# Kernel tuning notes

Hardware: AMD Instinct MI355X
Metric: run time of the kernel (lower is better)

Reference implementation:

```python
import jax, jax.numpy as jnp
import numpy as np

N_USER = 250_000
N_ITEM = 250_000
E = 500_000
IN, H, C = 128, 64, 2
NEG_SLOPE = 0.01  # torch F.leaky_relu default


def setup_inputs() -> dict:
    key = jax.random.key(0)
    ks = jax.random.split(key, 24)
    d = {}
    d["feat_user"] = jax.random.normal(ks[0], (N_USER, IN), jnp.float32)
    d["feat_item"] = jax.random.normal(ks[1], (N_ITEM, IN), jnp.float32)
    # per-etype linear params, layer 1 (in_feats -> h_dim)
    s1 = 1.0 / np.sqrt(IN)
    d["W1_follows"] = jax.random.normal(ks[2], (IN, H), jnp.float32) * s1
    d["b1_follows"] = jax.random.normal(ks[3], (H,), jnp.float32) * s1
    d["W1_clicks"]  = jax.random.normal(ks[4], (IN, H), jnp.float32) * s1
    d["b1_clicks"]  = jax.random.normal(ks[5], (H,), jnp.float32) * s1
    d["W1_rev"]     = jax.random.normal(ks[6], (IN, H), jnp.float32) * s1
    d["b1_rev"]     = jax.random.normal(ks[7], (H,), jnp.float32) * s1
    # per-etype linear params, layer 2 (h_dim -> num_classes)
    s2 = 1.0 / np.sqrt(H)
    d["W2_follows"] = jax.random.normal(ks[8], (H, C), jnp.float32) * s2
    d["b2_follows"] = jax.random.normal(ks[9], (C,), jnp.float32) * s2
    d["W2_clicks"]  = jax.random.normal(ks[10], (H, C), jnp.float32) * s2
    d["b2_clicks"]  = jax.random.normal(ks[11], (C,), jnp.float32) * s2
    d["W2_rev"]     = jax.random.normal(ks[12], (H, C), jnp.float32) * s2
    d["b2_rev"]     = jax.random.normal(ks[13], (C,), jnp.float32) * s2
    # edge lists: (src, dst) per canonical etype
    d["follows_src"] = jax.random.randint(ks[14], (E,), 0, N_USER, jnp.int32)  # user->user
    d["follows_dst"] = jax.random.randint(ks[15], (E,), 0, N_USER, jnp.int32)
    d["clicks_src"]  = jax.random.randint(ks[16], (E,), 0, N_USER, jnp.int32)  # user->item
    d["clicks_dst"]  = jax.random.randint(ks[17], (E,), 0, N_ITEM, jnp.int32)
    d["rev_src"]     = jax.random.randint(ks[18], (E,), 0, N_ITEM, jnp.int32)  # item->user
    d["rev_dst"]     = jax.random.randint(ks[19], (E,), 0, N_USER, jnp.int32)
    return d


def _mean_agg(Wh, src, dst, n_dst):
    # copy_u + mean: gather transformed src feats per edge, segment-mean onto dst
    m = Wh[src]                                                   # [E, d]
    s = jax.ops.segment_sum(m, dst, num_segments=n_dst)           # [n_dst, d]
    deg = jax.ops.segment_sum(jnp.ones_like(dst, Wh.dtype), dst, num_segments=n_dst)
    return s / jnp.maximum(deg, 1.0)[:, None]                     # 0 for deg-0 nodes (DGL fills 0)


def _layer(fu, fi, Wf, bf, Wc, bc, Wr, br,
           fsrc, fdst, csrc, cdst, rsrc, rdst):
    # per-etype linear on src features, per-etype mean, cross-etype 'sum'
    h_user = (_mean_agg(fu @ Wf + bf, fsrc, fdst, N_USER)
              + _mean_agg(fi @ Wr + br, rsrc, rdst, N_USER))
    h_item = _mean_agg(fu @ Wc + bc, csrc, cdst, N_ITEM)
    return h_user, h_item


def reference(feat_user, feat_item,
              W1_follows, b1_follows, W1_clicks, b1_clicks, W1_rev, b1_rev,
              W2_follows, b2_follows, W2_clicks, b2_clicks, W2_rev, b2_rev,
              follows_src, follows_dst, clicks_src, clicks_dst, rev_src, rev_dst):
    h1u, h1i = _layer(feat_user, feat_item,
                      W1_follows, b1_follows, W1_clicks, b1_clicks, W1_rev, b1_rev,
                      follows_src, follows_dst, clicks_src, clicks_dst, rev_src, rev_dst)
    h2u = jnp.where(h1u >= 0, h1u, NEG_SLOPE * h1u)
    h2i = jnp.where(h1i >= 0, h1i, NEG_SLOPE * h1i)
    out_u, out_i = _layer(h2u, h2i,
                          W2_follows, b2_follows, W2_clicks, b2_clicks, W2_rev, b2_rev,
                          follows_src, follows_dst, clicks_src, clicks_dst, rev_src, rev_dst)
    # (h_dict, h_dict_2) flattened per ntype
    return (out_u, out_i, h2u, h2i)
```

## Files before the change

### kernel.cpp

```cpp
#include <hip/hip_runtime.h>
#include <cstdio>

#define NU 250000
#define NI 250000
#define NE 500000
#define ND 250000
#define NB_SCAN 245
#define NR 8
#define RSZ 31250

typedef __attribute__((ext_vector_type(8))) short short8v;
typedef __attribute__((ext_vector_type(4))) float float4v;

__device__ inline unsigned short f2bf(float x) {
  unsigned int b = __float_as_uint(x);
  unsigned int r = (b + 0x7FFFu + ((b >> 16) & 1u)) >> 16;
  return (unsigned short)r;
}
__device__ inline float bf2f(unsigned short u) {
  return __uint_as_float(((unsigned int)u) << 16);
}

__device__ inline void async_copy16(const float* g, float* l) {
  __builtin_amdgcn_global_load_lds((const __attribute__((address_space(1))) void*)g,
                                   (__attribute__((address_space(3))) void*)l, 16, 0, 0);
}

__device__ inline void nt_store4(float* p, float a, float b, float c, float d) {
  float4v v; v.x = a; v.y = b; v.z = c; v.w = d;
  __builtin_nontemporal_store(v, (float4v*)p);
}

__global__ void hist3_kernel(const int* __restrict__ fdst, const int* __restrict__ cdst,
                             const int* __restrict__ rdst,
                             int* __restrict__ degf, int* __restrict__ degc, int* __restrict__ degr) {
  int i = blockIdx.x * blockDim.x + threadIdx.x;
  if (i < NE) {
    atomicAdd(&degf[fdst[i]], 1);
    atomicAdd(&degc[cdst[i]], 1);
    atomicAdd(&degr[rdst[i]], 1);
  }
}

__global__ void scan1_kernel(const int* __restrict__ deg0, const int* __restrict__ deg1,
                             const int* __restrict__ deg2, int* __restrict__ bsum) {
  const int* deg = blockIdx.y == 0 ? deg0 : (blockIdx.y == 1 ? deg1 : deg2);
  int* bs = bsum + blockIdx.y * 256;
  __shared__ int s[256];
  int b = blockIdx.x, t = threadIdx.x;
  int base = b * 1024 + t * 4;
  int v = 0;
  #pragma unroll
  for (int i = 0; i < 4; ++i) if (base + i < ND) v += deg[base + i];
  s[t] = v; __syncthreads();
  for (int off = 128; off > 0; off >>= 1) { if (t < off) s[t] += s[t + off]; __syncthreads(); }
  if (t == 0) bs[b] = s[0];
}

__global__ void scan3_kernel(const int* __restrict__ deg0, const int* __restrict__ deg1,
                             const int* __restrict__ deg2, const int* __restrict__ bsum,
                             int* __restrict__ offs0, int* __restrict__ offs1, int* __restrict__ offs2,
                             int* __restrict__ cur0, int* __restrict__ cur1, int* __restrict__ cur2) {
  int y = blockIdx.y;
  const int* deg = y == 0 ? deg0 : (y == 1 ? deg1 : deg2);
  int* offs = y == 0 ? offs0 : (y == 1 ? offs1 : offs2);
  int* cursor = y == 0 ? cur0 : (y == 1 ? cur1 : cur2);
  const int* bs = bsum + y * 256;
  __shared__ int sb[256];
  __shared__ int s[256];
  int b = blockIdx.x, t = threadIdx.x;

  sb[t] = (t < NB_SCAN) ? bs[t] : 0;
  __syncthreads();
  for (int off = 1; off < 256; off <<= 1) {
    int x = (t >= off) ? sb[t - off] : 0;
    __syncthreads();
    sb[t] += x;
    __syncthreads();
  }
  int blockbase = (b == 0) ? 0 : sb[b - 1];

  int base = b * 1024 + t * 4;
  int v[4]; int sum = 0;
  #pragma unroll
  for (int i = 0; i < 4; ++i) { v[i] = (base + i < ND) ? deg[base + i] : 0; sum += v[i]; }
  s[t] = sum; __syncthreads();
  for (int off = 1; off < 256; off <<= 1) {
    int x = (t >= off) ? s[t - off] : 0;
    __syncthreads();
    s[t] += x;
    __syncthreads();
  }
  int run = blockbase + s[t] - sum;
  #pragma unroll
  for (int i = 0; i < 4; ++i) {
    if (base + i < ND) { offs[base + i] = run; cursor[base + i] = run; run += v[i]; }
  }
  if (b == 0 && t == 0) offs[ND] = NE;
}

__global__ void bucket_part_kernel(const int* __restrict__ fsrc, const int* __restrict__ fdst,
                                   const int* __restrict__ csrc, const int* __restrict__ cdst,
                                   const int* __restrict__ rsrc, const int* __restrict__ rdst,
                                   int* __restrict__ curf, int* __restrict__ curc, int* __restrict__ curr,
                                   int* __restrict__ srtf, int* __restrict__ srtc, int* __restrict__ srtr) {
  const int r = blockIdx.x & (NR - 1);
  const int chunk = blockIdx.x >> 3;
  const int lo = r * RSZ, hi = lo + RSZ;
  const int base = chunk * 1024;
  #pragma unroll
  for (int i = 0; i < 4; ++i) {
    int e = base + i * 256 + threadIdx.x;
    if (e < NE) {
      int d0 = fdst[e]; int s0 = fsrc[e];
      if (d0 >= lo && d0 < hi) { int p = atomicAdd(&curf[d0], 1); srtf[p] = s0; }
      int d1 = cdst[e]; int s1 = csrc[e];
      if (d1 >= lo && d1 < hi) { int p = atomicAdd(&curc[d1], 1); srtc[p] = s1; }
      int d2 = rdst[e]; int s2 = rsrc[e];
      if (d2 >= lo && d2 < hi) { int p = atomicAdd(&curr[d2], 1); srtr[p] = s2; }
    }
  }
}

__global__ void prepw_kernel(const float* __restrict__ W0, const float* __restrict__ W1,
                             const float* __restrict__ W2, unsigned short* __restrict__ T) {
  int gt = blockIdx.x * 256 + threadIdx.x;
  int et = gt >> 10;
  int g = gt & 1023;
  int gl = g & 63;
  int jm = (g >> 6) & 3;
  int c = g >> 8;
  int kb = c * 32 + (gl >> 4) * 8;
  int col = jm * 16 + (gl & 15);
  const float* W = et == 0 ? W0 : (et == 1 ? W1 : W2);
  short8v u;
  #pragma unroll
  for (int i = 0; i < 8; ++i) u[i] = (short)f2bf(W[(kb + i) * 64 + col]);
  ((short8v*)T)[gt] = u;
}

template <bool TWO>
__device__ inline void gemm_persist(float (*sx)[64 * 128],
                                    const float* __restrict__ X, int n, int ntiles,
                                    const unsigned short* __restrict__ Ta, const float* __restrict__ ba,
                                    const unsigned short* __restrict__ Tb, const float* __restrict__ bb,
                                    unsigned short* __restrict__ Ya, unsigned short* __restrict__ Yb) {
  const int tid = threadIdx.x;
  const int lane = tid & 63;
  const int wave = tid >> 6;
  const int cb = (lane >> 4) * 4;

  short8v A[4][4], B[4][4];
  #pragma unroll
  for (int c = 0; c < 4; ++c) {
    #pragma unroll
    for (int jm = 0; jm < 4; ++jm) {
      A[c][jm] = ((const short8v*)Ta)[c * 256 + jm * 64 + lane];
      if constexpr (TWO) B[c][jm] = ((const short8v*)Tb)[c * 256 + jm * 64 + lane];
    }
  }
  float4 bias_a[4], bias_b[4];
  #pragma unroll
  for (int jm = 0; jm < 4; ++jm) {
    bias_a[jm] = *(const float4*)&ba[jm * 16 + cb];
    if constexpr (TWO) bias_b[jm] = *(const float4*)&bb[jm * 16 + cb];
  }

  const int nl = wave * 16 + (lane & 15);
  const int sw = nl & 7;

  int t = blockIdx.x;
  if (t >= ntiles) return;
  {
    #pragma unroll
    for (int j = 0; j < 8; ++j) {
      int idx = (wave * 8 + j) * 64 + lane;
      int row = idx >> 5, u = idx & 31;
      int gr = t * 64 + row; if (gr >= n) gr = n - 1;
      const float* src = X + (size_t)gr * 128 + ((u ^ (row & 7)) << 2);
      float* dst = &sx[0][(wave * 8 + j) * 256];
      async_copy16(src, dst);
    }
  }
  asm volatile("s_waitcnt vmcnt(0)" ::: "memory");
  __syncthreads();

  int cur = 0;
  while (true) {
    int tn = t + (int)gridDim.x;
    bool more = (tn < ntiles);
    if (more) {
      #pragma unroll
      for (int j = 0; j < 8; ++j) {
        int idx = (wave * 8 + j) * 64 + lane;
        int row = idx >> 5, u = idx & 31;
        int gr = tn * 64 + row; if (gr >= n) gr = n - 1;
        const float* src = X + (size_t)gr * 128 + ((u ^ (row & 7)) << 2);
        float* dst = &sx[cur ^ 1][(wave * 8 + j) * 256];
        async_copy16(src, dst);
      }
    }

    float4v accA[4] = {};
    float4v accB[4] = {};
    #pragma unroll
    for (int c = 0; c < 4; ++c) {
      int s0 = c * 8 + (lane >> 4) * 2;
      float4 f0 = *(const float4*)&sx[cur][nl * 128 + (((s0 + 0) ^ sw) << 2)];
      float4 f1 = *(const float4*)&sx[cur][nl * 128 + (((s0 + 1) ^ sw) << 2)];
      short8v bfr;
      bfr[0] = (short)f2bf(f0.x); bfr[1] = (short)f2bf(f0.y);
      bfr[2] = (short)f2bf(f0.z); bfr[3] = (short)f2bf(f0.w);
      bfr[4] = (short)f2bf(f1.x); bfr[5] = (short)f2bf(f1.y);
      bfr[6] = (short)f2bf(f1.z); bfr[7] = (short)f2bf(f1.w);
      #pragma unroll
      for (int jm = 0; jm < 4; ++jm) {
        accA[jm] = __builtin_amdgcn_mfma_f32_16x16x32_bf16(A[c][jm], bfr, accA[jm], 0, 0, 0);
        if constexpr (TWO)
          accB[jm] = __builtin_amdgcn_mfma_f32_16x16x32_bf16(B[c][jm], bfr, accB[jm], 0, 0, 0);
      }
    }
    int node = t * 64 + nl;
    if (node < n) {
      #pragma unroll
      for (int jm = 0; jm < 4; ++jm) {
        ushort4 o;
        o.x = f2bf(accA[jm][0] + bias_a[jm].x);
        o.y = f2bf(accA[jm][1] + bias_a[jm].y);
        o.z = f2bf(accA[jm][2] + bias_a[jm].z);
        o.w = f2bf(accA[jm][3] + bias_a[jm].w);
        *(ushort4*)&Ya[(size_t)node * 64 + jm * 16 + cb] = o;
        if constexpr (TWO) {
          ushort4 o2;
          o2.x = f2bf(accB[jm][0] + bias_b[jm].x);
          o2.y = f2bf(accB[jm][1] + bias_b[jm].y);
          o2.z = f2bf(accB[jm][2] + bias_b[jm].z);
          o2.w = f2bf(accB[jm][3] + bias_b[jm].w);
          *(ushort4*)&Yb[(size_t)node * 64 + jm * 16 + cb] = o2;
        }
      }
    }

    if (!more) break;
    asm volatile("s_waitcnt vmcnt(0)" ::: "memory");
    __syncthreads();
    cur ^= 1;
    t = tn;
  }
}

__global__ __launch_bounds__(256, 2) void gemm_both_kernel(
    const float* __restrict__ Xu, int un, int utiles,
    const float* __restrict__ Xi, int in_, int itiles,
    const unsigned short* __restrict__ Tf, const float* __restrict__ b1f,
    const unsigned short* __restrict__ Tc, const float* __restrict__ b1c,
    const unsigned short* __restrict__ Tr, const float* __restrict__ b1r,
    unsigned short* __restrict__ Whf, unsigned short* __restrict__ Whc,
    unsigned short* __restrict__ Whr) {
  __shared__ float sx[2][64 * 128];
  gemm_persist<true>(sx, Xu, un, utiles, Tf, b1f, Tc, b1c, Whf, Whc);
  __syncthreads();
  gemm_persist<false>(sx, Xi, in_, itiles, Tr, b1r, nullptr, nullptr, Whr, nullptr);
}

__global__ __launch_bounds__(256) void agg_fused_kernel(
    const unsigned short* __restrict__ Whf, const unsigned short* __restrict__ Whr,
    const unsigned short* __restrict__ Whc,
    const int* __restrict__ offs_f, const int* __restrict__ srt_f,
    const int* __restrict__ offs_r, const int* __restrict__ srt_r,
    const int* __restrict__ offs_c, const int* __restrict__ srt_c,
    const float* __restrict__ W2f, const float* __restrict__ b2f,
    const float* __restrict__ W2c, const float* __restrict__ b2c,
    const float* __restrict__ W2r, const float* __restrict__ b2r,
    float* __restrict__ h2u, float* __restrict__ h2i,
    float* __restrict__ Y2f, float* __restrict__ Y2c, float* __restrict__ Y2r,
    int ub) {
  const int tid = threadIdx.x;
  const int gid = tid >> 4;
  const int q = tid & 15;

  if (blockIdx.x < ub) {
    int d0 = (blockIdx.x * 16 + gid) * 2;
    int d1 = d0 + 1;
    bool v0 = d0 < NU, v1 = d1 < NU;
    int ef0 = v0 ? offs_f[d0] : 0, ef0e = v0 ? offs_f[d0 + 1] : 0;
    int ef1 = v1 ? offs_f[d1] : 0, ef1e = v1 ? offs_f[d1 + 1] : 0;
    int er0 = v0 ? offs_r[d0] : 0, er0e = v0 ? offs_r[d0 + 1] : 0;
    int er1 = v1 ? offs_r[d1] : 0, er1e = v1 ? offs_r[d1 + 1] : 0;
    float rf0 = 1.0f / fmaxf((float)(ef0e - ef0), 1.0f);
    float rf1 = 1.0f / fmaxf((float)(ef1e - ef1), 1.0f);
    float rr0 = 1.0f / fmaxf((float)(er0e - er0), 1.0f);
    float rr1 = 1.0f / fmaxf((float)(er1e - er1), 1.0f);

    float af0[4] = {0, 0, 0, 0}, af1[4] = {0, 0, 0, 0};
    float ar0[4] = {0, 0, 0, 0}, ar1[4] = {0, 0, 0, 0};
    while (ef0 < ef0e || ef1 < ef1e || er0 < er0e || er1 < er1e) {
      bool hf0 = ef0 < ef0e, hf1 = ef1 < ef1e, hr0 = er0 < er0e, hr1 = er1 < er1e;
      ushort4 vf0, vf1, vr0, vr1;
      if (hf0) { int s = srt_f[ef0]; vf0 = *(const ushort4*)&Whf[(size_t)s * 64 + q * 4]; }
      if (hf1) { int s = srt_f[ef1]; vf1 = *(const ushort4*)&Whf[(size_t)s * 64 + q * 4]; }
      if (hr0) { int s = srt_r[er0]; vr0 = *(const ushort4*)&Whr[(size_t)s * 64 + q * 4]; }
      if (hr1) { int s = srt_r[er1]; vr1 = *(const ushort4*)&Whr[(size_t)s * 64 + q * 4]; }
      if (hf0) { af0[0] += bf2f(vf0.x); af0[1] += bf2f(vf0.y); af0[2] += bf2f(vf0.z); af0[3] += bf2f(vf0.w); ++ef0; }
      if (hf1) { af1[0] += bf2f(vf1.x); af1[1] += bf2f(vf1.y); af1[2] += bf2f(vf1.z); af1[3] += bf2f(vf1.w); ++ef1; }
      if (hr0) { ar0[0] += bf2f(vr0.x); ar0[1] += bf2f(vr0.y); ar0[2] += bf2f(vr0.z); ar0[3] += bf2f(vr0.w); ++er0; }
      if (hr1) { ar1[0] += bf2f(vr1.x); ar1[1] += bf2f(vr1.y); ar1[2] += bf2f(vr1.z); ar1[3] += bf2f(vr1.w); ++er1; }
    }

    float h0v[4], h1v[4];
    #pragma unroll
    for (int i = 0; i < 4; ++i) {
      float x0 = af0[i] * rf0 + ar0[i] * rr0;
      h0v[i] = x0 >= 0.f ? x0 : 0.01f * x0;
      float x1 = af1[i] * rf1 + ar1[i] * rr1;
      h1v[i] = x1 >= 0.f ? x1 : 0.01f * x1;
    }
    if (v0) nt_store4(&h2u[(size_t)d0 * 64 + q * 4], h0v[0], h0v[1], h0v[2], h0v[3]);
    if (v1) nt_store4(&h2u[(size_t)d1 * 64 + q * 4], h1v[0], h1v[1], h1v[2], h1v[3]);

    float pf00 = 0, pf01 = 0, pc00 = 0, pc01 = 0;
    float pf10 = 0, pf11 = 0, pc10 = 0, pc11 = 0;
    #pragma unroll
    for (int i = 0; i < 4; ++i) {
      int j = q * 4 + i;
      float wf0 = W2f[j * 2 + 0], wf1 = W2f[j * 2 + 1];
      float wc0 = W2c[j * 2 + 0], wc1 = W2c[j * 2 + 1];
      pf00 += h0v[i] * wf0; pf01 += h0v[i] * wf1;
      pc00 += h0v[i] * wc0; pc01 += h0v[i] * wc1;
      pf10 += h1v[i] * wf0; pf11 += h1v[i] * wf1;
      pc10 += h1v[i] * wc0; pc11 += h1v[i] * wc1;
    }
    #pragma unroll
    for (int off = 1; off < 16; off <<= 1) {
      pf00 += __shfl_xor(pf00, off, 64); pf01 += __shfl_xor(pf01, off, 64);
      pc00 += __shfl_xor(pc00, off, 64); pc01 += __shfl_xor(pc01, off, 64);
      pf10 += __shfl_xor(pf10, off, 64); pf11 += __shfl_xor(pf11, off, 64);
      pc10 += __shfl_xor(pc10, off, 64); pc11 += __shfl_xor(pc11, off, 64);
    }
    if (q == 0) {
      if (v0) {
        __builtin_nontemporal_store(pf00 + b2f[0], &Y2f[(size_t)d0 * 2 + 0]);
        __builtin_nontemporal_store(pf01 + b2f[1], &Y2f[(size_t)d0 * 2 + 1]);
        __builtin_nontemporal_store(pc00 + b2c[0], &Y2c[(size_t)d0 * 2 + 0]);
        __builtin_nontemporal_store(pc01 + b2c[1], &Y2c[(size_t)d0 * 2 + 1]);
      }
      if (v1) {
        __builtin_nontemporal_store(pf10 + b2f[0], &Y2f[(size_t)d1 * 2 + 0]);
        __builtin_nontemporal_store(pf11 + b2f[1], &Y2f[(size_t)d1 * 2 + 1]);
        __builtin_nontemporal_store(pc10 + b2c[0], &Y2c[(size_t)d1 * 2 + 0]);
        __builtin_nontemporal_store(pc11 + b2c[1], &Y2c[(size_t)d1 * 2 + 1]);
      }
    }
  } else {
    int d0 = ((blockIdx.x - ub) * 16 + gid) * 2;
    int d1 = d0 + 1;
    bool v0 = d0 < NI, v1 = d1 < NI;
    int ec0 = v0 ? offs_c[d0] : 0, ec0e = v0 ? offs_c[d0 + 1] : 0;
    int ec1 = v1 ? offs_c[d1] : 0, ec1e = v1 ? offs_c[d1 + 1] : 0;
    float rc0 = 1.0f / fmaxf((float)(ec0e - ec0), 1.0f);
    float rc1 = 1.0f / fmaxf((float)(ec1e - ec1), 1.0f);

    float ac0[4] = {0, 0, 0, 0}, ac1[4] = {0, 0, 0, 0};
    while (ec0 < ec0e || ec1 < ec1e) {
      bool h0 = ec0 < ec0e, h1 = ec1 < ec1e;
      ushort4 v0v, v1v;
      if (h0) { int s = srt_c[ec0]; v0v = *(const ushort4*)&Whc[(size_t)s * 64 + q * 4]; }
      if (h1) { int s = srt_c[ec1]; v1v = *(const ushort4*)&Whc[(size_t)s * 64 + q * 4]; }
      if (h0) { ac0[0] += bf2f(v0v.x); ac0[1] += bf2f(v0v.y); ac0[2] += bf2f(v0v.z); ac0[3] += bf2f(v0v.w); ++ec0; }
      if (h1) { ac1[0] += bf2f(v1v.x); ac1[1] += bf2f(v1v.y); ac1[2] += bf2f(v1v.z); ac1[3] += bf2f(v1v.w); ++ec1; }
    }

    float h0v[4], h1v[4];
    #pragma unroll
    for (int i = 0; i < 4; ++i) {
      float x0 = ac0[i] * rc0;
      h0v[i] = x0 >= 0.f ? x0 : 0.01f * x0;
      float x1 = ac1[i] * rc1;
      h1v[i] = x1 >= 0.f ? x1 : 0.01f * x1;
    }
    if (v0) nt_store4(&h2i[(size_t)d0 * 64 + q * 4], h0v[0], h0v[1], h0v[2], h0v[3]);
    if (v1) nt_store4(&h2i[(size_t)d1 * 64 + q * 4], h1v[0], h1v[1], h1v[2], h1v[3]);

    float p00 = 0, p01 = 0, p10 = 0, p11 = 0;
    #pragma unroll
    for (int i = 0; i < 4; ++i) {
      int j = q * 4 + i;
      float w0 = W2r[j * 2 + 0], w1 = W2r[j * 2 + 1];
      p00 += h0v[i] * w0; p01 += h0v[i] * w1;
      p10 += h1v[i] * w0; p11 += h1v[i] * w1;
    }
    #pragma unroll
    for (int off = 1; off < 16; off <<= 1) {
      p00 += __shfl_xor(p00, off, 64); p01 += __shfl_xor(p01, off, 64);
      p10 += __shfl_xor(p10, off, 64); p11 += __shfl_xor(p11, off, 64);
    }
    if (q == 0) {
      if (v0) {
        __builtin_nontemporal_store(p00 + b2r[0], &Y2r[(size_t)d0 * 2 + 0]);
        __builtin_nontemporal_store(p01 + b2r[1], &Y2r[(size_t)d0 * 2 + 1]);
      }
      if (v1) {
        __builtin_nontemporal_store(p10 + b2r[0], &Y2r[(size_t)d1 * 2 + 0]);
        __builtin_nontemporal_store(p11 + b2r[1], &Y2r[(size_t)d1 * 2 + 1]);
      }
    }
  }
}

__global__ void out_fused_kernel(const float* __restrict__ Y2f, const float* __restrict__ Y2r,
                                 const float* __restrict__ Y2c,
                                 const int* __restrict__ offs_f, const int* __restrict__ srt_f,
                                 const int* __restrict__ offs_r, const int* __restrict__ srt_r,
                                 const int* __restrict__ offs_c, const int* __restrict__ srt_c,
                                 float* __restrict__ out_u, float* __restrict__ out_i, int ub) {
  if (blockIdx.x < ub) {
    int d = blockIdx.x * 256 + threadIdx.x;
    if (d >= NU) return;
    int f = offs_f[d], f1 = offs_f[d + 1];
    int r = offs_r[d], r1 = offs_r[d + 1];
    float rf = 1.0f / fmaxf((float)(f1 - f), 1.0f);
    float rr = 1.0f / fmaxf((float)(r1 - r), 1.0f);
    float a0 = 0.f, a1 = 0.f, c0 = 0.f, c1 = 0.f;
    while (f < f1 || r < r1) {
      bool hf = f < f1, hr = r < r1;
      float2 yf, yr;
      if (hf) { int s = srt_f[f]; yf = *(const float2*)&Y2f[(size_t)s * 2]; }
      if (hr) { int s = srt_r[r]; yr = *(const float2*)&Y2r[(size_t)s * 2]; }
      if (hf) { a0 += yf.x; a1 += yf.y; ++f; }
      if (hr) { c0 += yr.x; c1 += yr.y; ++r; }
    }
    __builtin_nontemporal_store(a0 * rf + c0 * rr, &out_u[(size_t)d * 2 + 0]);
    __builtin_nontemporal_store(a1 * rf + c1 * rr, &out_u[(size_t)d * 2 + 1]);
  } else {
    int d = (blockIdx.x - ub) * 256 + threadIdx.x;
    if (d >= NI) return;
    int c = offs_c[d], c1e = offs_c[d + 1];
    float rc = 1.0f / fmaxf((float)(c1e - c), 1.0f);
    float a0 = 0.f, a1 = 0.f;
    for (; c < c1e; ++c) {
      int s = srt_c[c];
      a0 += Y2c[(size_t)s * 2 + 0]; a1 += Y2c[(size_t)s * 2 + 1];
    }
    __builtin_nontemporal_store(a0 * rc, &out_i[(size_t)d * 2 + 0]);
    __builtin_nontemporal_store(a1 * rc, &out_i[(size_t)d * 2 + 1]);
  }
}

extern "C" void kernel_launch(void* const* d_in, const int* in_sizes, int n_in,
                              void* d_out, int out_size, void* d_ws, size_t ws_size,
                              hipStream_t stream) {
  const float* feat_user = (const float*)d_in[0];
  const float* feat_item = (const float*)d_in[1];
  const float* W1f = (const float*)d_in[2];  const float* b1f = (const float*)d_in[3];
  const float* W1c = (const float*)d_in[4];  const float* b1c = (const float*)d_in[5];
  const float* W1r = (const float*)d_in[6];  const float* b1r = (const float*)d_in[7];
  const float* W2f = (const float*)d_in[8];  const float* b2f = (const float*)d_in[9];
  const float* W2c = (const float*)d_in[10]; const float* b2c = (const float*)d_in[11];
  const float* W2r = (const float*)d_in[12]; const float* b2r = (const float*)d_in[13];
  const int* fsrc = (const int*)d_in[14];  const int* fdst = (const int*)d_in[15];
  const int* csrc = (const int*)d_in[16];  const int* cdst = (const int*)d_in[17];
  const int* rsrc = (const int*)d_in[18];  const int* rdst = (const int*)d_in[19];

  float* out = (float*)d_out;
  float* out_u = out;
  float* out_i = out + 2 * NU;
  float* h2u  = out + 1000000;
  float* h2i  = out + 17000000;

  unsigned short* Whf = (unsigned short*)d_ws;
  unsigned short* Whc = Whf + 16000000;
  unsigned short* Whr = Whc + 16000000;
  unsigned short* Wtab = Whr + 16000000;
  unsigned short* Tf = Wtab;
  unsigned short* Tc = Wtab + 8192;
  unsigned short* Tr = Wtab + 16384;
  int* ibase = (int*)(Wtab + 24576);
  const int P = 250304;
  int* offs_f = ibase;            int* offs_c = offs_f + P;  int* offs_r = offs_c + P;
  int* cur_f  = offs_r + P;       int* cur_c  = cur_f + P;   int* cur_r  = cur_c + P;
  int* deg_f  = cur_r + P;        int* deg_c  = deg_f + P;   int* deg_r  = deg_c + P;
  int* srt_f  = deg_r + P;
  int* srt_c  = srt_f + 500096;
  int* srt_r  = srt_c + 500096;
  int* bsum   = srt_r + 500096;
  float* Y2f  = (float*)(bsum + 768);
  float* Y2c  = Y2f + 500000;
  float* Y2r  = Y2c + 500000;

  size_t need = 96000000ull + 24576ull * 2ull
              + (9ull * P + 3ull * 500096ull + 768ull + 1500000ull) * 4ull;
  if (ws_size < need) {
    fprintf(stderr, "kernel_launch: ws too small (%zu < %zu)\n", ws_size, need);
    return;
  }

  (void)hipMemsetAsync(deg_f, 0, (size_t)(3 * P) * 4, stream);

  const int eb = (NE + 255) / 256;

  prepw_kernel<<<12, 256, 0, stream>>>(W1f, W1c, W1r, Wtab);

  const int utiles = (NU + 63) / 64;
  const int itiles = (NI + 63) / 64;
  gemm_both_kernel<<<512, 256, 0, stream>>>(feat_user, NU, utiles, feat_item, NI, itiles,
                                            Tf, b1f, Tc, b1c, Tr, b1r, Whf, Whc, Whr);

  hist3_kernel<<<eb, 256, 0, stream>>>(fdst, cdst, rdst, deg_f, deg_c, deg_r);
  scan1_kernel<<<dim3(NB_SCAN, 3), 256, 0, stream>>>(deg_f, deg_c, deg_r, bsum);
  scan3_kernel<<<dim3(NB_SCAN, 3), 256, 0, stream>>>(deg_f, deg_c, deg_r, bsum,
                                                     offs_f, offs_c, offs_r,
                                                     cur_f, cur_c, cur_r);
  const int chunks = (NE + 1023) / 1024;
  bucket_part_kernel<<<chunks * NR, 256, 0, stream>>>(fsrc, fdst, csrc, cdst, rsrc, rdst,
                                                      cur_f, cur_c, cur_r, srt_f, srt_c, srt_r);

  const int ub = (NU + 31) / 32;
  agg_fused_kernel<<<2 * ub, 256, 0, stream>>>(Whf, Whr, Whc,
                                               offs_f, srt_f, offs_r, srt_r, offs_c, srt_c,
                                               W2f, b2f, W2c, b2c, W2r, b2r,
                                               h2u, h2i, Y2f, Y2c, Y2r, ub);

  const int ob = (NU + 255) / 256;
  out_fused_kernel<<<2 * ob, 256, 0, stream>>>(Y2f, Y2r, Y2c,
                                               offs_f, srt_f, offs_r, srt_r, offs_c, srt_c,
                                               out_u, out_i, ob);
}
```

Baseline: 324.4 us.

## Stage GEMM output through LDS for coalesced stores, relax waitcnt, range-partition histogram

```diff
diff --git a/kernel.cpp b/kernel.cpp
--- a/kernel.cpp
+++ b/kernel.cpp
@@ -31,14 +31,24 @@
   __builtin_nontemporal_store(v, (float4v*)p);
 }
 
-__global__ void hist3_kernel(const int* __restrict__ fdst, const int* __restrict__ cdst,
-                             const int* __restrict__ rdst,
-                             int* __restrict__ degf, int* __restrict__ degc, int* __restrict__ degr) {
-  int i = blockIdx.x * blockDim.x + threadIdx.x;
-  if (i < NE) {
-    atomicAdd(&degf[fdst[i]], 1);
-    atomicAdd(&degc[cdst[i]], 1);
-    atomicAdd(&degr[rdst[i]], 1);
+__global__ void hist_part_kernel(const int* __restrict__ fdst, const int* __restrict__ cdst,
+                                 const int* __restrict__ rdst,
+                                 int* __restrict__ degf, int* __restrict__ degc, int* __restrict__ degr) {
+  const int r = blockIdx.x & (NR - 1);
+  const int chunk = blockIdx.x >> 3;
+  const int lo = r * RSZ, hi = lo + RSZ;
+  const int base = chunk * 1024;
+  #pragma unroll
+  for (int i = 0; i < 4; ++i) {
+    int e = base + i * 256 + threadIdx.x;
+    if (e < NE) {
+      int d0 = fdst[e];
+      if (d0 >= lo && d0 < hi) atomicAdd(&degf[d0], 1);
+      int d1 = cdst[e];
+      if (d1 >= lo && d1 < hi) atomicAdd(&degc[d1], 1);
+      int d2 = rdst[e];
+      if (d2 >= lo && d2 < hi) atomicAdd(&degr[d2], 1);
+    }
   }
 }
 
@@ -220,30 +230,59 @@
           accB[jm] = __builtin_amdgcn_mfma_f32_16x16x32_bf16(B[c][jm], bfr, accB[jm], 0, 0, 0);
       }
     }
-    int node = t * 64 + nl;
-    if (node < n) {
+
+    __syncthreads();
+    unsigned short* trA = (unsigned short*)&sx[cur][0];
+    unsigned short* trB = trA + 4096;
+    #pragma unroll
+    for (int jm = 0; jm < 4; ++jm) {
+      int s = jm * 4 + (lane >> 4);
+      ushort4 o;
+      o.x = f2bf(accA[jm][0] + bias_a[jm].x);
+      o.y = f2bf(accA[jm][1] + bias_a[jm].y);
+      o.z = f2bf(accA[jm][2] + bias_a[jm].z);
+      o.w = f2bf(accA[jm][3] + bias_a[jm].w);
+      *(ushort4*)&trA[nl * 64 + ((s ^ (nl & 15)) * 4)] = o;
+      if constexpr (TWO) {
+        ushort4 o2;
+        o2.x = f2bf(accB[jm][0] + bias_b[jm].x);
+        o2.y = f2bf(accB[jm][1] + bias_b[jm].y);
+        o2.z = f2bf(accB[jm][2] + bias_b[jm].z);
+        o2.w = f2bf(accB[jm][3] + bias_b[jm].w);
+        *(ushort4*)&trB[nl * 64 + ((s ^ (nl & 15)) * 4)] = o2;
+      }
+    }
+    __syncthreads();
+
+    #pragma unroll
+    for (int it = 0; it < 4; ++it) {
+      int u = it * 256 + tid;
+      int nrow = u >> 4, s = u & 15;
+      int node = t * 64 + nrow;
+      if (node < n) {
+        uint2 v = *(const uint2*)&trA[nrow * 64 + ((s ^ (nrow & 15)) * 4)];
+        *(uint2*)&Ya[(size_t)node * 64 + s * 4] = v;
+      }
+    }
+    if constexpr (TWO) {
       #pragma unroll
-      for (int jm = 0; jm < 4; ++jm) {
-        ushort4 o;
-        o.x = f2bf(accA[jm][0] + bias_a[jm].x);
-        o.y = f2bf(accA[jm][1] + bias_a[jm].y);
-        o.z = f2bf(accA[jm][2] + bias_a[jm].z);
-        o.w = f2bf(accA[jm][3] + bias_a[jm].w);
-        *(ushort4*)&Ya[(size_t)node * 64 + jm * 16 + cb] = o;
-        if constexpr (TWO) {
-          ushort4 o2;
-          o2.x = f2bf(accB[jm][0] + bias_b[jm].x);
-          o2.y = f2bf(accB[jm][1] + bias_b[jm].y);
-          o2.z = f2bf(accB[jm][2] + bias_b[jm].z);
-          o2.w = f2bf(accB[jm][3] + bias_b[jm].w);
-          *(ushort4*)&Yb[(size_t)node * 64 + jm * 16 + cb] = o2;
+      for (int it = 0; it < 4; ++it) {
+        int u = it * 256 + tid;
+        int nrow = u >> 4, s = u & 15;
+        int node = t * 64 + nrow;
+        if (node < n) {
+          uint2 v = *(const uint2*)&trB[nrow * 64 + ((s ^ (nrow & 15)) * 4)];
+          *(uint2*)&Yb[(size_t)node * 64 + s * 4] = v;
         }
       }
     }
 
     if (!more) break;
-    asm volatile("s_waitcnt vmcnt(0)" ::: "memory");
-    __syncthreads();
+    if constexpr (TWO) asm volatile("s_waitcnt vmcnt(8)" ::: "memory");
+    else               asm volatile("s_waitcnt vmcnt(4)" ::: "memory");
+    __builtin_amdgcn_sched_barrier(0);
+    __builtin_amdgcn_s_barrier();
+    __builtin_amdgcn_sched_barrier(0);
     cur ^= 1;
     t = tn;
   }
@@ -496,8 +535,6 @@
 
   (void)hipMemsetAsync(deg_f, 0, (size_t)(3 * P) * 4, stream);
 
-  const int eb = (NE + 255) / 256;
-
   prepw_kernel<<<12, 256, 0, stream>>>(W1f, W1c, W1r, Wtab);
 
   const int utiles = (NU + 63) / 64;
@@ -505,12 +542,12 @@
   gemm_both_kernel<<<512, 256, 0, stream>>>(feat_user, NU, utiles, feat_item, NI, itiles,
                                             Tf, b1f, Tc, b1c, Tr, b1r, Whf, Whc, Whr);
 
-  hist3_kernel<<<eb, 256, 0, stream>>>(fdst, cdst, rdst, deg_f, deg_c, deg_r);
+  const int chunks = (NE + 1023) / 1024;
+  hist_part_kernel<<<chunks * NR, 256, 0, stream>>>(fdst, cdst, rdst, deg_f, deg_c, deg_r);
   scan1_kernel<<<dim3(NB_SCAN, 3), 256, 0, stream>>>(deg_f, deg_c, deg_r, bsum);
   scan3_kernel<<<dim3(NB_SCAN, 3), 256, 0, stream>>>(deg_f, deg_c, deg_r, bsum,
                                                      offs_f, offs_c, offs_r,
                                                      cur_f, cur_c, cur_r);
-  const int chunks = (NE + 1023) / 1024;
   bucket_part_kernel<<<chunks * NR, 256, 0, stream>>>(fsrc, fdst, csrc, cdst, rsrc, rdst,
                                                       cur_f, cur_c, cur_r, srt_f, srt_c, srt_r);
 
```

Result: slower. 340.6 us (+5.0%).
